# Kernel tuning notes

Measured on AMD Instinct MI355X. Metric: run time of the kernel, lower is better.

Reference implementation:

```python
import jax, jax.numpy as jnp
import numpy as np

B, S, D = 1, 2048, 1024
H, DK = 16, 64
DFF, E, K = 4096, 8, 2
EPS = float(np.finfo(np.float32).eps)  # torch nn.RMSNorm default eps = finfo.eps


def setup_inputs() -> dict:
    key = jax.random.key(0)
    ks = jax.random.split(key, 8)
    s = 0.02
    return {
        "x": jax.random.normal(ks[0], (B, S, D), jnp.float32),
        "qkv_w": jax.random.normal(ks[1], (3 * D, D), jnp.float32) * s,
        "out_w": jax.random.normal(ks[2], (D, D), jnp.float32) * s,
        "router_w": jax.random.normal(ks[3], (E, D), jnp.float32) * s,
        "w1": jax.random.normal(ks[4], (E, DFF, D), jnp.float32) * s,
        "w2": jax.random.normal(ks[5], (E, D, DFF), jnp.float32) * s,
        "norm1_w": jnp.ones((D,), jnp.float32),
        "norm2_w": jnp.ones((D,), jnp.float32),
    }


def _rmsnorm(x, w):
    return x * jax.lax.rsqrt(jnp.mean(x * x, axis=-1, keepdims=True) + EPS) * w


def _rope(x):
    # x: [B, S, H, dk]; rotate-half RoPE as in RotaryPositionalEmbedding
    dk = x.shape[-1]
    inv_freq = 1.0 / (10000.0 ** (jnp.arange(0, dk, 2, dtype=jnp.float32) / dk))
    t = jnp.arange(x.shape[1], dtype=jnp.float32)
    freqs = t[:, None] * inv_freq[None, :]          # [S, dk/2]
    cos = jnp.cos(freqs)[None, :, None, :]
    sin = jnp.sin(freqs)[None, :, None, :]
    x1, x2 = jnp.split(x, 2, axis=-1)
    return jnp.concatenate([x1 * cos - x2 * sin, x2 * cos + x1 * sin], axis=-1)


def _block(x, qkv_w, out_w, router_w, w1, w2, norm1_w, norm2_w):
    Bv, Sv, Dv = x.shape
    # --- attention with RoPE (causal, eval mode) ---
    h = _rmsnorm(x, norm1_w)
    qkv = (h @ qkv_w.T).reshape(Bv, Sv, 3, H, DK)
    q, k, v = qkv[:, :, 0], qkv[:, :, 1], qkv[:, :, 2]   # [B,S,H,dk]
    q = _rope(q)
    k = _rope(k)
    scores = jnp.einsum('bshd,bthd->bhst', q, k) / np.float32(np.sqrt(DK))
    causal = jnp.tril(jnp.ones((Sv, Sv), dtype=bool))
    scores = jnp.where(causal, scores, jnp.float32(-jnp.inf))
    attn = jax.nn.softmax(scores, axis=-1)
    o = jnp.einsum('bhst,bthd->bshd', attn, v).reshape(Bv, Sv, Dv)
    x = x + o @ out_w.T
    # --- MoE with top-k routing ---
    h2 = _rmsnorm(x, norm2_w).reshape(-1, Dv)            # [T, D]
    logits = h2 @ router_w.T                             # [T, E]
    probs = jax.nn.softmax(logits, axis=-1)
    top_p, top_i = jax.lax.top_k(probs, K)               # [T, K]
    top_p = top_p / jnp.sum(top_p, axis=-1, keepdims=True)
    T = h2.shape[0]
    # dense per-token per-expert combine weights (same math as masked loop)
    w_dense = jnp.zeros((T, E), h2.dtype).at[jnp.arange(T)[:, None], top_i].add(top_p)
    hid = jax.nn.gelu(jnp.einsum('td,efd->etf', h2, w1), approximate=False)  # [E,T,DFF]
    eo = jnp.einsum('etf,edf->etd', hid, w2)                                  # [E,T,D]
    moe = jnp.einsum('etd,te->td', eo, w_dense).reshape(Bv, Sv, Dv)
    aux_loss = E * jnp.sum(jnp.mean(probs, axis=0) ** 2)
    return x + moe, aux_loss


def reference(x, qkv_w, out_w, router_w, w1, w2, norm1_w, norm2_w):
    return _block(x, qkv_w, out_w, router_w, w1, w2, norm1_w, norm2_w)
```

## Files before the change

### kernel.cpp

```cpp
#include <hip/hip_runtime.h>
#include <cstdint>
#include <math.h>

typedef float f32x4 __attribute__((ext_vector_type(4)));
typedef __bf16 bf16x8 __attribute__((ext_vector_type(8)));
typedef unsigned short us4 __attribute__((ext_vector_type(4)));

#define DEV static __device__ __forceinline__

DEV unsigned short f2bf(float f){
  union { __bf16 h; unsigned short u; } cv; cv.h = (__bf16)f; return cv.u;
}
DEV float bf2f(unsigned short u){ return __uint_as_float((unsigned int)u << 16); }

DEV void gload16(const void* g, void* l){
  __builtin_amdgcn_global_load_lds((__attribute__((address_space(1))) void*)g,
                                   (__attribute__((address_space(3))) void*)l, 16, 0, 0);
}

__global__ __launch_bounds__(256) void rmsnorm_kernel(const float* __restrict__ x, const float* __restrict__ w,
    unsigned short* __restrict__ ob){
  int t = blockIdx.x, tid = threadIdx.x;
  float4 xv = *(const float4*)(x + (long long)t*1024 + tid*4);
  float ss = xv.x*xv.x + xv.y*xv.y + xv.z*xv.z + xv.w*xv.w;
  for (int m=32;m;m>>=1) ss += __shfl_xor(ss,m);
  __shared__ float lds[4];
  if ((tid&63)==0) lds[tid>>6] = ss;
  __syncthreads();
  float tot = lds[0]+lds[1]+lds[2]+lds[3];
  float inv = rsqrtf(tot*(1.0f/1024.0f) + 1.1920928955078125e-07f);
  float4 wv = *(const float4*)(w + tid*4);
  us4 rb = { f2bf(xv.x*inv*wv.x), f2bf(xv.y*inv*wv.y), f2bf(xv.z*inv*wv.z), f2bf(xv.w*inv*wv.w) };
  *(us4*)&ob[(long long)t*1024 + tid*4] = rb;
}

__global__ __launch_bounds__(256) void rmsnorm2_kernel(const float* __restrict__ xp, int ksn, long long kstride,
    const float* __restrict__ w, float* __restrict__ x1, unsigned short* __restrict__ hb, float* __restrict__ hf){
  int t = blockIdx.x, tid = threadIdx.x;
  long long b = (long long)t*1024 + tid*4;
  float4 xv = {0.f,0.f,0.f,0.f};
  for (int ks=0; ks<ksn; ++ks){
    float4 a = *(const float4*)(xp + ks*kstride + b);
    xv.x+=a.x; xv.y+=a.y; xv.z+=a.z; xv.w+=a.w;
  }
  *(float4*)(x1 + b) = xv;
  float ss = xv.x*xv.x + xv.y*xv.y + xv.z*xv.z + xv.w*xv.w;
  for (int m=32;m;m>>=1) ss += __shfl_xor(ss,m);
  __shared__ float lds[4];
  if ((tid&63)==0) lds[tid>>6] = ss;
  __syncthreads();
  float tot = lds[0]+lds[1]+lds[2]+lds[3];
  float inv = rsqrtf(tot*(1.0f/1024.0f) + 1.1920928955078125e-07f);
  float4 wv = *(const float4*)(w + tid*4);
  float r0 = xv.x*inv*wv.x, r1 = xv.y*inv*wv.y, r2 = xv.z*inv*wv.z, r3 = xv.w*inv*wv.w;
  us4 rb = { f2bf(r0), f2bf(r1), f2bf(r2), f2bf(r3) };
  *(us4*)&hb[b] = rb;
  float4 rf; rf.x=r0; rf.y=r1; rf.z=r2; rf.w=r3;
  *(float4*)(hf + b) = rf;
}

template<int EPI, bool GATHER>
__global__ __launch_bounds__(256) void gemm_bt(
    const unsigned short* __restrict__ A, int lda,
    const float* __restrict__ Bw, long long bstride, int ldb,
    int M, int N, int K, int KS, long long ksoff,
    const int* __restrict__ counts, const int* __restrict__ offs,
    const int* __restrict__ tok_list, const float* __restrict__ wgt,
    const float* __restrict__ resid,
    float* __restrict__ Cf, unsigned short* __restrict__ Cb, int ldc)
{
  const int z = blockIdx.z;
  const int e = z / KS, ks = z - e*KS;
  const int Me = counts ? counts[e] : M;
  const int by = blockIdx.y;
  if (by * 128 >= Me) return;
  const int rbase = offs ? offs[e] : 0;
  const int bx = blockIdx.x;
  const float* B = Bw + (long long)e * bstride;
  const int kn = K / KS;
  const int kbeg = ks * kn;
  const int nt = kn >> 5;

  __shared__ __align__(16) char smem[49152];

  const int tid = threadIdx.x, lane = tid & 63, w = tid >> 6;
  const int wr = w >> 1, wc = w & 1;

  const unsigned short* asrc[2];
  #pragma unroll
  for (int i = 0; i < 2; ++i){
    int G = tid + i*256;
    int R = G >> 2, c = G & 3;
    int cg = c ^ ((R>>1)&3);
    int lr = by*128 + R; if (lr >= Me) lr = Me-1;
    int li = rbase + lr;
    int ar = GATHER ? (tok_list[li] >> 1) : li;
    asrc[i] = A + (long long)ar * lda + kbeg + cg*8;
  }
  const float* bsrc[4];
  #pragma unroll
  for (int i = 0; i < 4; ++i){
    int G = tid + i*256;
    int R = G >> 3, c = G & 7;
    int cg = c ^ (R & 7);
    bsrc[i] = B + (long long)(bx*128 + R) * ldb + kbeg + cg*4;
  }

  f32x4 acc[4][4] = {};

  auto stage = [&](int b, int kof){
    char* s = smem + b*24576;
    #pragma unroll
    for (int i = 0; i < 2; ++i) gload16(asrc[i] + kof, s + (i*256 + w*64)*16);
    #pragma unroll
    for (int i = 0; i < 4; ++i) gload16(bsrc[i] + kof, s + 8192 + (i*256 + w*64)*16);
  };

  stage(0, 0);
  __syncthreads();

  for (int t = 0; t < nt; ++t){
    int cur = t & 1;
    if (t + 1 < nt) stage(cur ^ 1, (t+1)*32);
    const char* abase = smem + cur*24576;
    const char* bbase = abase + 8192;
    bf16x8 af[4], bfr[4];
    #pragma unroll
    for (int m=0;m<4;++m){
      int R = wr*64 + m*16 + (lane&15);
      int c = (lane>>4) ^ ((R>>1)&3);
      af[m] = *(const bf16x8*)(abase + R*64 + c*16);
    }
    #pragma unroll
    for (int n=0;n<4;++n){
      int R = wc*64 + n*16 + (lane&15);
      int c0 = ((lane>>4)*2) ^ (R&7);
      int c1 = c0 ^ 1;
      f32x4 v0 = *(const f32x4*)(bbase + R*128 + c0*16);
      f32x4 v1 = *(const f32x4*)(bbase + R*128 + c1*16);
      bf16x8 tt;
      tt[0]=(__bf16)v0[0]; tt[1]=(__bf16)v0[1]; tt[2]=(__bf16)v0[2]; tt[3]=(__bf16)v0[3];
      tt[4]=(__bf16)v1[0]; tt[5]=(__bf16)v1[1]; tt[6]=(__bf16)v1[2]; tt[7]=(__bf16)v1[3];
      bfr[n] = tt;
    }
    #pragma unroll
    for (int m=0;m<4;++m)
      #pragma unroll
      for (int n=0;n<4;++n)
        acc[m][n] = __builtin_amdgcn_mfma_f32_16x16x32_bf16(af[m], bfr[n], acc[m][n], 0, 0, 0);
    __syncthreads();
  }

  #pragma unroll
  for (int m=0;m<4;++m){
    #pragma unroll
    for (int r=0;r<4;++r){
      int lr = by*128 + wr*64 + m*16 + 4*(lane>>4) + r;
      if (lr >= Me) continue;
      #pragma unroll
      for (int n=0;n<4;++n){
        int col = bx*128 + wc*64 + n*16 + (lane&15);
        float v = acc[m][n][r];
        if constexpr (EPI == 1){
          if (ks == 0) v += resid[(long long)lr*ldc + col];
          Cf[ks*ksoff + (long long)lr*ldc + col] = v;
        } else if constexpr (EPI == 2){
          float g = 0.5f * v * (1.0f + erff(v * 0.70710678118654752f));
          Cb[(long long)(rbase+lr)*ldc + col] = f2bf(g);
        } else if constexpr (EPI == 3){
          int gi = rbase + lr;
          int ts = tok_list[gi];
          Cf[ks*ksoff + (long long)ts*ldc + col] = v * wgt[gi];
        } else {
          Cb[(long long)lr*ldc + col] = f2bf(v);
        }
      }
    }
  }
}

__global__ __launch_bounds__(256) void rope_kernel(const unsigned short* __restrict__ qkvb,
    unsigned short* __restrict__ q, unsigned short* __restrict__ k){
  int t = blockIdx.x, tid = threadIdx.x;
  const unsigned short* row = qkvb + (long long)t*3072;
  #pragma unroll
  for (int u2=0; u2<2; ++u2){
    int pid = tid + u2*256;
    int hh = pid >> 5, j = pid & 31;
    float invf = __expf(-(float)j * 0.28782313662425575f);
    float fr = (float)t * invf;
    float sn, cs;
    __sincosf(fr, &sn, &cs);
    int base = hh*64 + j;
    long long ob_ = (long long)t*1024 + base;
    float a = bf2f(row[base]), b = bf2f(row[base+32]);
    q[ob_]    = f2bf(a*cs - b*sn);
    q[ob_+32] = f2bf(b*cs + a*sn);
    a = bf2f(row[1024+base]); b = bf2f(row[1024+base+32]);
    k[ob_]    = f2bf(a*cs - b*sn);
    k[ob_+32] = f2bf(b*cs + a*sn);
  }
}

__global__ __launch_bounds__(256) void attn_kernel(
    const unsigned short* __restrict__ Q,
    const unsigned short* __restrict__ K,
    const unsigned short* __restrict__ V, int ldv,
    unsigned short* __restrict__ O)
{
  const int bx = blockIdx.x, h = blockIdx.y;
  const int q0 = bx*64;
  const int tid = threadIdx.x, lane = tid&63, w = tid>>6;

  __shared__ __align__(16) unsigned short Ks[64*64];
  __shared__ __align__(16) unsigned short Vs[64*64];
  __shared__ __align__(16) unsigned short Ps[4*16*64];
  unsigned short* Pw = Ps + w*1024;

  const int qrow = q0 + w*16 + (lane&15);
  bf16x8 aq[2];
  #pragma unroll
  for (int kk=0;kk<2;++kk)
    aq[kk] = *(const bf16x8*)&Q[(long long)qrow*1024 + h*64 + 32*kk + 8*(lane>>4)];

  f32x4 o[4] = {};
  float Mx[4] = {-INFINITY,-INFINITY,-INFINITY,-INFINITY};
  float Ls[4] = {0.f,0.f,0.f,0.f};

  const int row_g = q0 + w*16 + 4*(lane>>4);
  const int nt = bx + 1;
  for (int it = 0; it < nt; ++it){
    int k0 = it*64;
    #pragma unroll
    for (int i=0;i<2;++i){
      int seg = 4*i + w;
      int row = seg*8 + (lane>>3);
      int cs = (lane&7) ^ (row&7);
      gload16(&K[(long long)(k0+row)*1024 + h*64 + cs*8], &Ks[seg*512]);
      gload16(&V[(long long)(k0+row)*ldv  + h*64 + cs*8], &Vs[seg*512]);
    }
    __syncthreads();
    f32x4 st[4];
    #pragma unroll
    for (int kt=0;kt<4;++kt){
      f32x4 s = {0.f,0.f,0.f,0.f};
      #pragma unroll
      for (int kk=0;kk<2;++kk){
        int R = kt*16 + (lane&15);
        int ch = ((lane>>4)+4*kk) ^ (R&7);
        bf16x8 bk = *(const bf16x8*)&Ks[R*64 + ch*8];
        s = __builtin_amdgcn_mfma_f32_16x16x32_bf16(aq[kk], bk, s, 0,0,0);
      }
      st[kt] = s;
    }
    #pragma unroll
    for (int kt=0;kt<4;++kt){
      int col = k0 + kt*16 + (lane&15);
      #pragma unroll
      for (int r=0;r<4;++r){
        float vv = st[kt][r]*0.125f;
        st[kt][r] = (col <= row_g + r) ? vv : -INFINITY;
      }
    }
    float sf[4];
    #pragma unroll
    for (int r=0;r<4;++r){
      float mx = fmaxf(fmaxf(st[0][r],st[1][r]),fmaxf(st[2][r],st[3][r]));
      mx = fmaxf(mx, __shfl_xor(mx,1));
      mx = fmaxf(mx, __shfl_xor(mx,2));
      mx = fmaxf(mx, __shfl_xor(mx,4));
      mx = fmaxf(mx, __shfl_xor(mx,8));
      float mn = fmaxf(Mx[r], mx);
      float sc = __expf(Mx[r]-mn);
      Mx[r]=mn; sf[r]=sc;
      float ls=0.f;
      #pragma unroll
      for (int kt=0;kt<4;++kt){ float pp = __expf(st[kt][r]-mn); st[kt][r]=pp; ls+=pp; }
      Ls[r] = Ls[r]*sc + ls;
    }
    #pragma unroll
    for (int dt=0;dt<4;++dt)
      #pragma unroll
      for (int r=0;r<4;++r) o[dt][r] *= sf[r];
    #pragma unroll
    for (int kt=0;kt<4;++kt)
      #pragma unroll
      for (int r=0;r<4;++r){
        int prow = 4*(lane>>4)+r, pcol = kt*16+(lane&15);
        int byteoff = (prow*128 + pcol*2) ^ ((prow&7)<<4);
        *(unsigned short*)((char*)Pw + byteoff) = f2bf(st[kt][r]);
      }
    bf16x8 pa[2];
    #pragma unroll
    for (int kk=0;kk<2;++kk){
      int pr = lane&15;
      int ch = ((lane>>4)+4*kk) ^ (pr&7);
      pa[kk] = *(const bf16x8*)&Pw[pr*64 + ch*8];
    }
    #pragma unroll
    for (int dt=0;dt<4;++dt){
      #pragma unroll
      for (int kk=0;kk<2;++kk){
        union { unsigned short u[8]; bf16x8 v; } Ub;
        #pragma unroll
        for (int j=0;j<8;++j){
          int kr = 32*kk + 8*(lane>>4) + j;
          int d = dt*16 + (lane&15);
          int byteoff = (kr*128 + d*2) ^ ((kr&7)<<4);
          Ub.u[j] = *(const unsigned short*)((const char*)Vs + byteoff);
        }
        o[dt] = __builtin_amdgcn_mfma_f32_16x16x32_bf16(pa[kk], Ub.v, o[dt], 0,0,0);
      }
    }
    __syncthreads();
  }
  #pragma unroll
  for (int r=0;r<4;++r){
    float l = Ls[r];
    l += __shfl_xor(l,1); l += __shfl_xor(l,2); l += __shfl_xor(l,4); l += __shfl_xor(l,8);
    Ls[r] = 1.0f / l;
  }
  #pragma unroll
  for (int dt=0;dt<4;++dt)
    #pragma unroll
    for (int r=0;r<4;++r){
      float vv = o[dt][r]*Ls[r];
      int rg = row_g + r;
      O[(long long)rg*1024 + h*64 + dt*16 + (lane&15)] = f2bf(vv);
    }
}

__global__ __launch_bounds__(256) void router_kernel(const float* __restrict__ h2f, const float* __restrict__ rw,
    float* __restrict__ probs, int* __restrict__ tope, float* __restrict__ topw, int* __restrict__ counts){
  int t = blockIdx.x, tid = threadIdx.x;
  float4 hv = *(const float4*)(h2f + (long long)t*1024 + tid*4);
  float pe[8];
  #pragma unroll
  for (int e2=0;e2<8;++e2){
    float4 wv = *(const float4*)(rw + e2*1024 + tid*4);
    pe[e2] = hv.x*wv.x + hv.y*wv.y + hv.z*wv.z + hv.w*wv.w;
  }
  __shared__ float lds[32];
  #pragma unroll
  for (int e2=0;e2<8;++e2){
    float v = pe[e2];
    for (int m=32;m;m>>=1) v += __shfl_xor(v,m);
    if ((tid&63)==0) lds[(tid>>6)*8+e2] = v;
  }
  __syncthreads();
  if (tid==0){
    float lg[8], pp[8];
    #pragma unroll
    for (int e2=0;e2<8;++e2) lg[e2] = lds[e2]+lds[8+e2]+lds[16+e2]+lds[24+e2];
    float mx = lg[0];
    for (int e2=1;e2<8;++e2) mx = fmaxf(mx, lg[e2]);
    float s = 0.f;
    for (int e2=0;e2<8;++e2){ pp[e2] = __expf(lg[e2]-mx); s += pp[e2]; }
    float inv = 1.0f/s;
    int i0 = 0;
    for (int e2=1;e2<8;++e2) if (pp[e2] > pp[i0]) i0 = e2;
    int i1 = (i0==0)?1:0;
    for (int e2=0;e2<8;++e2) if (e2!=i0 && pp[e2] > pp[i1]) i1 = e2;
    for (int e2=0;e2<8;++e2) probs[t*8+e2] = pp[e2]*inv;
    float p0 = pp[i0], p1 = pp[i1], wsum = p0+p1;
    tope[t*2] = i0; tope[t*2+1] = i1;
    topw[t*2] = p0/wsum; topw[t*2+1] = p1/wsum;
    atomicAdd(&counts[i0],1); atomicAdd(&counts[i1],1);
  }
}

__global__ void init_kernel(int* counts, int* cursor){
  int i = threadIdx.x;
  if (i<8){ counts[i]=0; cursor[i]=0; }
}

__global__ void prefix_kernel(const int* counts, int* offs){
  if (threadIdx.x==0){
    int a=0;
    for (int e2=0;e2<8;++e2){ offs[e2]=a; a+=counts[e2]; }
  }
}

__global__ void scatter_kernel(const int* __restrict__ tope, const float* __restrict__ topw,
    const int* __restrict__ offs, int* __restrict__ cursor, int* __restrict__ tok_list, float* __restrict__ wgt){
  int t = blockIdx.x*blockDim.x + threadIdx.x;
  if (t >= 2048) return;
  #pragma unroll
  for (int s=0;s<2;++s){
    int e2 = tope[t*2+s];
    int pos = atomicAdd(&cursor[e2], 1);
    int i = offs[e2] + pos;
    tok_list[i] = t*2+s;
    wgt[i] = topw[t*2+s];
  }
}

__global__ __launch_bounds__(256) void aux_kernel(const float* __restrict__ probs, float* __restrict__ out){
  int tid = threadIdx.x;
  float pe[8] = {0,0,0,0,0,0,0,0};
  for (int t = tid; t < 2048; t += 256){
    #pragma unroll
    for (int e2=0;e2<8;++e2) pe[e2] += probs[t*8+e2];
  }
  __shared__ float lds[32];
  #pragma unroll
  for (int e2=0;e2<8;++e2){
    float v = pe[e2];
    for (int m=32;m;m>>=1) v += __shfl_xor(v,m);
    if ((tid&63)==0) lds[(tid>>6)*8 + e2] = v;
  }
  __syncthreads();
  if (tid==0){
    float aux = 0.f;
    #pragma unroll
    for (int e2=0;e2<8;++e2){
      float mean = (lds[e2]+lds[8+e2]+lds[16+e2]+lds[24+e2]) * (1.0f/2048.0f);
      aux += mean*mean;
    }
    out[2097152] = 8.0f * aux;
  }
}

__global__ __launch_bounds__(256) void final_kernel(const float* __restrict__ x1, const float* __restrict__ slots,
    int ksn, long long kstride, float* __restrict__ out){
  int t = blockIdx.x, tid = threadIdx.x;
  long long b = (long long)t*1024 + tid*4;
  float4 a = *(const float4*)(x1 + b);
  long long s = (long long)t*2048 + tid*4;
  for (int ks=0; ks<ksn; ++ks){
    float4 s0 = *(const float4*)(slots + ks*kstride + s);
    float4 s1 = *(const float4*)(slots + ks*kstride + s + 1024);
    a.x += s0.x + s1.x; a.y += s0.y + s1.y; a.z += s0.z + s1.z; a.w += s0.w + s1.w;
  }
  *(float4*)(out + b) = a;
}

extern "C" void kernel_launch(void* const* d_in, const int* in_sizes, int n_in,
                              void* d_out, int out_size, void* d_ws, size_t ws_size,
                              hipStream_t stream)
{
  (void)in_sizes; (void)n_in; (void)out_size;
  const float* x    = (const float*)d_in[0];
  const float* qkvw = (const float*)d_in[1];
  const float* outw = (const float*)d_in[2];
  const float* rw   = (const float*)d_in[3];
  const float* w1   = (const float*)d_in[4];
  const float* w2   = (const float*)d_in[5];
  const float* n1w  = (const float*)d_in[6];
  const float* n2w  = (const float*)d_in[7];
  float* out = (float*)d_out;

  char* base = (char*)d_ws;
  const size_t MB = 1ull<<20;
  const bool big = ws_size >= 150*MB;
  const int KSO = big ? 4 : 2;
  const int KSW = big ? 4 : 2;

  unsigned short* h_b  = (unsigned short*)(base + 0*MB);
  unsigned short* qb   = (unsigned short*)(base + 4*MB);
  unsigned short* kb   = (unsigned short*)(base + 8*MB);
  unsigned short* ob   = (unsigned short*)(base + 12*MB);
  unsigned short* qkvb = (unsigned short*)(base + 16*MB);
  unsigned short* hid  = (unsigned short*)(base + 0*MB);

  float *x1p, *h2f, *slots, *x1;
  unsigned short* h2b;
  char* small_;
  if (big){
    x1p   = (float*)(base + 32*MB);
    h2f   = (float*)(base + 64*MB);
    slots = (float*)(base + 72*MB);
    x1    = (float*)(base + 136*MB);
    h2b   = (unsigned short*)(base + 144*MB);
    small_ = base + 148*MB;
  } else {
    x1p   = (float*)(base + 32*MB);
    h2f   = (float*)(base + 48*MB);
    slots = (float*)(base + 32*MB);
    x1    = (float*)(base + 64*MB);
    h2b   = (unsigned short*)(base + 72*MB);
    small_ = base + 76*MB;
  }
  float* probs = (float*)(small_);
  int*   tope  = (int*)(small_ + 256*1024);
  float* topw  = (float*)(small_ + 512*1024);
  int*   tok_list = (int*)(small_ + 768*1024);
  float* wgt   = (float*)(small_ + 1024*1024);
  int*   counts= (int*)(small_ + 1536*1024);
  int*   offs  = (int*)(small_ + 1536*1024 + 256);
  int*   cursor= (int*)(small_ + 1536*1024 + 512);

  init_kernel<<<1,64,0,stream>>>(counts, cursor);
  rmsnorm_kernel<<<2048,256,0,stream>>>(x, n1w, h_b);
  gemm_bt<4,false><<<dim3(24,16,1),256,0,stream>>>(h_b,1024, qkvw,0,1024, 2048,3072,1024, 1,0,
      nullptr,nullptr,nullptr,nullptr,nullptr, nullptr,qkvb,3072);
  rope_kernel<<<2048,256,0,stream>>>(qkvb, qb, kb);
  attn_kernel<<<dim3(32,16),256,0,stream>>>(qb, kb, qkvb+2048, 3072, ob);
  gemm_bt<1,false><<<dim3(8,16,KSO),256,0,stream>>>(ob,1024, outw,0,1024, 2048,1024,1024, KSO,(long long)2048*1024,
      nullptr,nullptr,nullptr,nullptr, x, x1p,nullptr,1024);
  rmsnorm2_kernel<<<2048,256,0,stream>>>(x1p, KSO, (long long)2048*1024, n2w, x1, h2b, h2f);
  router_kernel<<<2048,256,0,stream>>>(h2f, rw, probs, tope, topw, counts);
  prefix_kernel<<<1,64,0,stream>>>(counts, offs);
  scatter_kernel<<<8,256,0,stream>>>(tope, topw, offs, cursor, tok_list, wgt);
  gemm_bt<2,true><<<dim3(32,16,8),256,0,stream>>>(h2b,1024, w1,(long long)4096*1024,1024, 2048,4096,1024, 1,0,
      counts,offs,tok_list,nullptr,nullptr, nullptr,hid,4096);
  gemm_bt<3,false><<<dim3(8,16,8*KSW),256,0,stream>>>(hid,4096, w2,(long long)4096*1024,4096, 2048,1024,4096, KSW,(long long)4096*1024,
      counts,offs,tok_list,wgt,nullptr, slots,nullptr,1024);
  aux_kernel<<<1,256,0,stream>>>(probs, out);
  final_kernel<<<2048,256,0,stream>>>(x1, slots, KSW, (long long)4096*1024, out);
}
```

Measured before the change: 452.9 us.

## Replace LDS-staged GEMM with direct global-load streaming GEMM and XCD-aware block remap

The double-buffered LDS GEMM, which used async global-to-LDS loads and a barrier per k-step, is replaced by a kernel where each wave loads its A and B fragments straight from global memory into registers. The output tile changes from 128x128 to 64x256, with each wave owning a 64-column strip. Block indices are remapped so consecutive tiles land on the same XCD, which should improve L2 locality. This removes the LDS traffic and barriers, but it gives up on-chip sharing of operands between waves, so the kernel now depends on L1/L2 hit rates and more global load instructions.

Result: slower. 867.6 us (+91.6%).

```diff
diff --git a/kernel.cpp b/kernel.cpp
--- a/kernel.cpp
+++ b/kernel.cpp
@@ -60,7 +60,7 @@
 }
 
 template<int EPI, bool GATHER>
-__global__ __launch_bounds__(256) void gemm_bt(
+__global__ __launch_bounds__(256) void gemm_stream(
     const unsigned short* __restrict__ A, int lda,
     const float* __restrict__ Bw, long long bstride, int ldb,
     int M, int N, int K, int KS, long long ksoff,
@@ -69,75 +69,56 @@
     const float* __restrict__ resid,
     float* __restrict__ Cf, unsigned short* __restrict__ Cb, int ldc)
 {
-  const int z = blockIdx.z;
+  const int gx = gridDim.x, gy = gridDim.y;
+  int flat = blockIdx.x + gx*(blockIdx.y + gy*blockIdx.z);
+  int nwg = gx*gy*gridDim.z;
+  int q = nwg >> 3, r = nwg & 7;
+  int xcd = flat & 7, p = flat >> 3;
+  int nf = (xcd < r ? xcd*(q+1) : r*(q+1) + (xcd-r)*q) + p;
+  const int by = nf % gx;
+  int rest = nf / gx;
+  const int bx = rest % gy;
+  const int z  = rest / gy;
+
   const int e = z / KS, ks = z - e*KS;
   const int Me = counts ? counts[e] : M;
-  const int by = blockIdx.y;
-  if (by * 128 >= Me) return;
+  if (by * 64 >= Me) return;
   const int rbase = offs ? offs[e] : 0;
-  const int bx = blockIdx.x;
   const float* B = Bw + (long long)e * bstride;
-  const int kn = K / KS;
-  const int kbeg = ks * kn;
-  const int nt = kn >> 5;
-
-  __shared__ __align__(16) char smem[49152];
-
-  const int tid = threadIdx.x, lane = tid & 63, w = tid >> 6;
-  const int wr = w >> 1, wc = w & 1;
-
-  const unsigned short* asrc[2];
-  #pragma unroll
-  for (int i = 0; i < 2; ++i){
-    int G = tid + i*256;
-    int R = G >> 2, c = G & 3;
-    int cg = c ^ ((R>>1)&3);
-    int lr = by*128 + R; if (lr >= Me) lr = Me-1;
+  const int kbeg = ks * (K/KS);
+  const int nt = (K/KS) >> 5;
+
+  const int lane = threadIdx.x & 63, w = threadIdx.x >> 6;
+  const int l15 = lane & 15, l4 = lane >> 4;
+
+  const unsigned short* arow[4];
+  #pragma unroll
+  for (int m=0;m<4;++m){
+    int lr = by*64 + m*16 + l15; if (lr >= Me) lr = Me-1;
     int li = rbase + lr;
     int ar = GATHER ? (tok_list[li] >> 1) : li;
-    asrc[i] = A + (long long)ar * lda + kbeg + cg*8;
-  }
-  const float* bsrc[4];
-  #pragma unroll
-  for (int i = 0; i < 4; ++i){
-    int G = tid + i*256;
-    int R = G >> 3, c = G & 7;
-    int cg = c ^ (R & 7);
-    bsrc[i] = B + (long long)(bx*128 + R) * ldb + kbeg + cg*4;
+    arow[m] = A + (long long)ar*lda + kbeg + l4*8;
+  }
+  const float* brow[4];
+  #pragma unroll
+  for (int n=0;n<4;++n){
+    int R = bx*256 + w*64 + n*16 + l15;
+    brow[n] = B + (long long)R*ldb + kbeg + l4*8;
   }
 
   f32x4 acc[4][4] = {};
 
-  auto stage = [&](int b, int kof){
-    char* s = smem + b*24576;
-    #pragma unroll
-    for (int i = 0; i < 2; ++i) gload16(asrc[i] + kof, s + (i*256 + w*64)*16);
-    #pragma unroll
-    for (int i = 0; i < 4; ++i) gload16(bsrc[i] + kof, s + 8192 + (i*256 + w*64)*16);
-  };
-
-  stage(0, 0);
-  __syncthreads();
-
+  #pragma unroll 2
   for (int t = 0; t < nt; ++t){
-    int cur = t & 1;
-    if (t + 1 < nt) stage(cur ^ 1, (t+1)*32);
-    const char* abase = smem + cur*24576;
-    const char* bbase = abase + 8192;
-    bf16x8 af[4], bfr[4];
-    #pragma unroll
-    for (int m=0;m<4;++m){
-      int R = wr*64 + m*16 + (lane&15);
-      int c = (lane>>4) ^ ((R>>1)&3);
-      af[m] = *(const bf16x8*)(abase + R*64 + c*16);
-    }
+    const int k0 = t*32;
+    bf16x8 af[4];
+    #pragma unroll
+    for (int m=0;m<4;++m) af[m] = *(const bf16x8*)(arow[m] + k0);
+    bf16x8 bfr[4];
     #pragma unroll
     for (int n=0;n<4;++n){
-      int R = wc*64 + n*16 + (lane&15);
-      int c0 = ((lane>>4)*2) ^ (R&7);
-      int c1 = c0 ^ 1;
-      f32x4 v0 = *(const f32x4*)(bbase + R*128 + c0*16);
-      f32x4 v1 = *(const f32x4*)(bbase + R*128 + c1*16);
+      f32x4 v0 = *(const f32x4*)(brow[n] + k0);
+      f32x4 v1 = *(const f32x4*)(brow[n] + k0 + 4);
       bf16x8 tt;
       tt[0]=(__bf16)v0[0]; tt[1]=(__bf16)v0[1]; tt[2]=(__bf16)v0[2]; tt[3]=(__bf16)v0[3];
       tt[4]=(__bf16)v1[0]; tt[5]=(__bf16)v1[1]; tt[6]=(__bf16)v1[2]; tt[7]=(__bf16)v1[3];
@@ -148,19 +129,18 @@
       #pragma unroll
       for (int n=0;n<4;++n)
         acc[m][n] = __builtin_amdgcn_mfma_f32_16x16x32_bf16(af[m], bfr[n], acc[m][n], 0, 0, 0);
-    __syncthreads();
   }
 
   #pragma unroll
   for (int m=0;m<4;++m){
     #pragma unroll
-    for (int r=0;r<4;++r){
-      int lr = by*128 + wr*64 + m*16 + 4*(lane>>4) + r;
+    for (int r2=0;r2<4;++r2){
+      int lr = by*64 + m*16 + 4*l4 + r2;
       if (lr >= Me) continue;
       #pragma unroll
       for (int n=0;n<4;++n){
-        int col = bx*128 + wc*64 + n*16 + (lane&15);
-        float v = acc[m][n][r];
+        int col = bx*256 + w*64 + n*16 + l15;
+        float v = acc[m][n][r2];
         if constexpr (EPI == 1){
           if (ks == 0) v += resid[(long long)lr*ldc + col];
           Cf[ks*ksoff + (long long)lr*ldc + col] = v;
@@ -492,19 +472,19 @@
 
   init_kernel<<<1,64,0,stream>>>(counts, cursor);
   rmsnorm_kernel<<<2048,256,0,stream>>>(x, n1w, h_b);
-  gemm_bt<4,false><<<dim3(24,16,1),256,0,stream>>>(h_b,1024, qkvw,0,1024, 2048,3072,1024, 1,0,
+  gemm_stream<4,false><<<dim3(32,12,1),256,0,stream>>>(h_b,1024, qkvw,0,1024, 2048,3072,1024, 1,0,
       nullptr,nullptr,nullptr,nullptr,nullptr, nullptr,qkvb,3072);
   rope_kernel<<<2048,256,0,stream>>>(qkvb, qb, kb);
   attn_kernel<<<dim3(32,16),256,0,stream>>>(qb, kb, qkvb+2048, 3072, ob);
-  gemm_bt<1,false><<<dim3(8,16,KSO),256,0,stream>>>(ob,1024, outw,0,1024, 2048,1024,1024, KSO,(long long)2048*1024,
+  gemm_stream<1,false><<<dim3(32,4,KSO),256,0,stream>>>(ob,1024, outw,0,1024, 2048,1024,1024, KSO,(long long)2048*1024,
       nullptr,nullptr,nullptr,nullptr, x, x1p,nullptr,1024);
   rmsnorm2_kernel<<<2048,256,0,stream>>>(x1p, KSO, (long long)2048*1024, n2w, x1, h2b, h2f);
   router_kernel<<<2048,256,0,stream>>>(h2f, rw, probs, tope, topw, counts);
   prefix_kernel<<<1,64,0,stream>>>(counts, offs);
   scatter_kernel<<<8,256,0,stream>>>(tope, topw, offs, cursor, tok_list, wgt);
-  gemm_bt<2,true><<<dim3(32,16,8),256,0,stream>>>(h2b,1024, w1,(long long)4096*1024,1024, 2048,4096,1024, 1,0,
+  gemm_stream<2,true><<<dim3(32,16,8),256,0,stream>>>(h2b,1024, w1,(long long)4096*1024,1024, 2048,4096,1024, 1,0,
       counts,offs,tok_list,nullptr,nullptr, nullptr,hid,4096);
-  gemm_bt<3,false><<<dim3(8,16,8*KSW),256,0,stream>>>(hid,4096, w2,(long long)4096*1024,4096, 2048,1024,4096, KSW,(long long)4096*1024,
+  gemm_stream<3,false><<<dim3(32,4,8*KSW),256,0,stream>>>(hid,4096, w2,(long long)4096*1024,4096, 2048,1024,4096, KSW,(long long)4096*1024,
       counts,offs,tok_list,wgt,nullptr, slots,nullptr,1024);
   aux_kernel<<<1,256,0,stream>>>(probs, out);
   final_kernel<<<2048,256,0,stream>>>(x1, slots, KSW, (long long)4096*1024, out);
```

## Pre-convert weights to bf16 and use a bf16-bf16 GEMM with K=64 tiles

Applied to the files above, without the earlier changes.

Adds a conversion kernel that turns the fp32 weight matrices into bf16 in workspace before each GEMM. The GEMM then loads bf16 for both operands with 64-wide K tiles, instead of staging fp32 B and converting in registers. This is meant to cut the LDS footprint and conversion ALU work inside the GEMM. In exchange it adds extra full-weight passes each call, and replaces double-buffered staging with a single buffer and two barriers per step. It also fixes the split-K factors and the workspace layout, dropping the small-workspace fallback.

Result: faster. 436.5 us (-3.6%).

```diff
diff --git a/kernel.cpp b/kernel.cpp
--- a/kernel.cpp
+++ b/kernel.cpp
@@ -5,6 +5,7 @@
 typedef float f32x4 __attribute__((ext_vector_type(4)));
 typedef __bf16 bf16x8 __attribute__((ext_vector_type(8)));
 typedef unsigned short us4 __attribute__((ext_vector_type(4)));
+typedef unsigned short us8 __attribute__((ext_vector_type(8)));
 
 #define DEV static __device__ __forceinline__
 
@@ -16,6 +17,17 @@
 DEV void gload16(const void* g, void* l){
   __builtin_amdgcn_global_load_lds((__attribute__((address_space(1))) void*)g,
                                    (__attribute__((address_space(3))) void*)l, 16, 0, 0);
+}
+
+__global__ __launch_bounds__(256) void conv_kernel(const float* __restrict__ src,
+    unsigned short* __restrict__ dst, int n8){
+  int i = blockIdx.x*256 + threadIdx.x;
+  if (i >= n8) return;
+  float4 a = ((const float4*)src)[2*i];
+  float4 b = ((const float4*)src)[2*i+1];
+  us8 o = { f2bf(a.x), f2bf(a.y), f2bf(a.z), f2bf(a.w),
+            f2bf(b.x), f2bf(b.y), f2bf(b.z), f2bf(b.w) };
+  ((us8*)dst)[i] = o;
 }
 
 __global__ __launch_bounds__(256) void rmsnorm_kernel(const float* __restrict__ x, const float* __restrict__ w,
@@ -60,9 +72,9 @@
 }
 
 template<int EPI, bool GATHER>
-__global__ __launch_bounds__(256) void gemm_bt(
+__global__ __launch_bounds__(256) void gemm_bb(
     const unsigned short* __restrict__ A, int lda,
-    const float* __restrict__ Bw, long long bstride, int ldb,
+    const unsigned short* __restrict__ Bb, long long bstride, int ldb,
     int M, int N, int K, int KS, long long ksoff,
     const int* __restrict__ counts, const int* __restrict__ offs,
     const int* __restrict__ tok_list, const float* __restrict__ wgt,
@@ -76,91 +88,74 @@
   if (by * 128 >= Me) return;
   const int rbase = offs ? offs[e] : 0;
   const int bx = blockIdx.x;
-  const float* B = Bw + (long long)e * bstride;
+  const unsigned short* B = Bb + (long long)e * bstride;
   const int kn = K / KS;
   const int kbeg = ks * kn;
-  const int nt = kn >> 5;
-
-  __shared__ __align__(16) char smem[49152];
+
+  __shared__ __align__(16) unsigned short As[128*64];
+  __shared__ __align__(16) unsigned short Bs[128*64];
 
   const int tid = threadIdx.x, lane = tid & 63, w = tid >> 6;
   const int wr = w >> 1, wc = w & 1;
-
-  const unsigned short* asrc[2];
-  #pragma unroll
-  for (int i = 0; i < 2; ++i){
-    int G = tid + i*256;
-    int R = G >> 2, c = G & 3;
-    int cg = c ^ ((R>>1)&3);
+  const int l15 = lane & 15, l4 = lane >> 4;
+
+  const unsigned short* asrc[4];
+  const unsigned short* bsrc[4];
+  #pragma unroll
+  for (int j=0;j<4;++j){
+    int G = j*256 + tid;
+    int R = G >> 3, c = G & 7;
+    int sc = c ^ (R & 7);
     int lr = by*128 + R; if (lr >= Me) lr = Me-1;
     int li = rbase + lr;
     int ar = GATHER ? (tok_list[li] >> 1) : li;
-    asrc[i] = A + (long long)ar * lda + kbeg + cg*8;
-  }
-  const float* bsrc[4];
-  #pragma unroll
-  for (int i = 0; i < 4; ++i){
-    int G = tid + i*256;
-    int R = G >> 3, c = G & 7;
-    int cg = c ^ (R & 7);
-    bsrc[i] = B + (long long)(bx*128 + R) * ldb + kbeg + cg*4;
+    asrc[j] = A + (long long)ar*lda + kbeg + sc*8;
+    bsrc[j] = B + (long long)(bx*128 + R)*ldb + kbeg + sc*8;
   }
 
   f32x4 acc[4][4] = {};
 
-  auto stage = [&](int b, int kof){
-    char* s = smem + b*24576;
-    #pragma unroll
-    for (int i = 0; i < 2; ++i) gload16(asrc[i] + kof, s + (i*256 + w*64)*16);
-    #pragma unroll
-    for (int i = 0; i < 4; ++i) gload16(bsrc[i] + kof, s + 8192 + (i*256 + w*64)*16);
-  };
-
-  stage(0, 0);
-  __syncthreads();
-
-  for (int t = 0; t < nt; ++t){
-    int cur = t & 1;
-    if (t + 1 < nt) stage(cur ^ 1, (t+1)*32);
-    const char* abase = smem + cur*24576;
-    const char* bbase = abase + 8192;
-    bf16x8 af[4], bfr[4];
-    #pragma unroll
-    for (int m=0;m<4;++m){
-      int R = wr*64 + m*16 + (lane&15);
-      int c = (lane>>4) ^ ((R>>1)&3);
-      af[m] = *(const bf16x8*)(abase + R*64 + c*16);
-    }
-    #pragma unroll
-    for (int n=0;n<4;++n){
-      int R = wc*64 + n*16 + (lane&15);
-      int c0 = ((lane>>4)*2) ^ (R&7);
-      int c1 = c0 ^ 1;
-      f32x4 v0 = *(const f32x4*)(bbase + R*128 + c0*16);
-      f32x4 v1 = *(const f32x4*)(bbase + R*128 + c1*16);
-      bf16x8 tt;
-      tt[0]=(__bf16)v0[0]; tt[1]=(__bf16)v0[1]; tt[2]=(__bf16)v0[2]; tt[3]=(__bf16)v0[3];
-      tt[4]=(__bf16)v1[0]; tt[5]=(__bf16)v1[1]; tt[6]=(__bf16)v1[2]; tt[7]=(__bf16)v1[3];
-      bfr[n] = tt;
-    }
-    #pragma unroll
-    for (int m=0;m<4;++m)
-      #pragma unroll
-      for (int n=0;n<4;++n)
-        acc[m][n] = __builtin_amdgcn_mfma_f32_16x16x32_bf16(af[m], bfr[n], acc[m][n], 0, 0, 0);
+  for (int k0 = 0; k0 < kn; k0 += 64){
     __syncthreads();
+    #pragma unroll
+    for (int j=0;j<4;++j){
+      gload16(asrc[j] + k0, &As[(j*256+tid)*8]);
+      gload16(bsrc[j] + k0, &Bs[(j*256+tid)*8]);
+    }
+    __syncthreads();
+    #pragma unroll
+    for (int kk=0;kk<2;++kk){
+      bf16x8 af[4], bfr[4];
+      #pragma unroll
+      for (int m=0;m<4;++m){
+        int R = wr*64 + m*16 + l15;
+        int c = (l4 + 4*kk) ^ (R&7);
+        af[m] = *(const bf16x8*)&As[R*64 + c*8];
+      }
+      #pragma unroll
+      for (int n=0;n<4;++n){
+        int R = wc*64 + n*16 + l15;
+        int c = (l4 + 4*kk) ^ (R&7);
+        bfr[n] = *(const bf16x8*)&Bs[R*64 + c*8];
+      }
+      #pragma unroll
+      for (int m=0;m<4;++m)
+        #pragma unroll
+        for (int n=0;n<4;++n)
+          acc[m][n] = __builtin_amdgcn_mfma_f32_16x16x32_bf16(af[m], bfr[n], acc[m][n], 0, 0, 0);
+    }
   }
 
   #pragma unroll
   for (int m=0;m<4;++m){
     #pragma unroll
-    for (int r=0;r<4;++r){
-      int lr = by*128 + wr*64 + m*16 + 4*(lane>>4) + r;
+    for (int r2=0;r2<4;++r2){
+      int lr = by*128 + wr*64 + m*16 + 4*l4 + r2;
       if (lr >= Me) continue;
       #pragma unroll
       for (int n=0;n<4;++n){
-        int col = bx*128 + wc*64 + n*16 + (lane&15);
-        float v = acc[m][n][r];
+        int col = bx*128 + wc*64 + n*16 + l15;
+        float v = acc[m][n][r2];
         if constexpr (EPI == 1){
           if (ks == 0) v += resid[(long long)lr*ldc + col];
           Cf[ks*ksoff + (long long)lr*ldc + col] = v;
@@ -439,7 +434,7 @@
                               void* d_out, int out_size, void* d_ws, size_t ws_size,
                               hipStream_t stream)
 {
-  (void)in_sizes; (void)n_in; (void)out_size;
+  (void)in_sizes; (void)n_in; (void)out_size; (void)ws_size;
   const float* x    = (const float*)d_in[0];
   const float* qkvw = (const float*)d_in[1];
   const float* outw = (const float*)d_in[2];
@@ -452,9 +447,8 @@
 
   char* base = (char*)d_ws;
   const size_t MB = 1ull<<20;
-  const bool big = ws_size >= 150*MB;
-  const int KSO = big ? 4 : 2;
-  const int KSW = big ? 4 : 2;
+  const int KSO = 4;
+  const int KSW = 2;
 
   unsigned short* h_b  = (unsigned short*)(base + 0*MB);
   unsigned short* qb   = (unsigned short*)(base + 4*MB);
@@ -463,24 +457,17 @@
   unsigned short* qkvb = (unsigned short*)(base + 16*MB);
   unsigned short* hid  = (unsigned short*)(base + 0*MB);
 
-  float *x1p, *h2f, *slots, *x1;
-  unsigned short* h2b;
-  char* small_;
-  if (big){
-    x1p   = (float*)(base + 32*MB);
-    h2f   = (float*)(base + 64*MB);
-    slots = (float*)(base + 72*MB);
-    x1    = (float*)(base + 136*MB);
-    h2b   = (unsigned short*)(base + 144*MB);
-    small_ = base + 148*MB;
-  } else {
-    x1p   = (float*)(base + 32*MB);
-    h2f   = (float*)(base + 48*MB);
-    slots = (float*)(base + 32*MB);
-    x1    = (float*)(base + 64*MB);
-    h2b   = (unsigned short*)(base + 72*MB);
-    small_ = base + 76*MB;
-  }
+  unsigned short* wbq = (unsigned short*)(base + 32*MB);
+  unsigned short* wbo = (unsigned short*)(base + 40*MB);
+  unsigned short* wb  = (unsigned short*)(base + 32*MB);
+
+  float* x1p   = (float*)(base + 96*MB);
+  float* slots = (float*)(base + 96*MB);
+  float* h2f   = (float*)(base + 128*MB);
+  float* x1    = (float*)(base + 136*MB);
+  unsigned short* h2b = (unsigned short*)(base + 144*MB);
+  char* small_ = base + 148*MB;
+
   float* probs = (float*)(small_);
   int*   tope  = (int*)(small_ + 256*1024);
   float* topw  = (float*)(small_ + 512*1024);
@@ -492,19 +479,23 @@
 
   init_kernel<<<1,64,0,stream>>>(counts, cursor);
   rmsnorm_kernel<<<2048,256,0,stream>>>(x, n1w, h_b);
-  gemm_bt<4,false><<<dim3(24,16,1),256,0,stream>>>(h_b,1024, qkvw,0,1024, 2048,3072,1024, 1,0,
+  conv_kernel<<<1536,256,0,stream>>>(qkvw, wbq, 3*1024*1024/8);
+  conv_kernel<<<512,256,0,stream>>>(outw, wbo, 1024*1024/8);
+  gemm_bb<4,false><<<dim3(24,16,1),256,0,stream>>>(h_b,1024, wbq,0,1024, 2048,3072,1024, 1,0,
       nullptr,nullptr,nullptr,nullptr,nullptr, nullptr,qkvb,3072);
   rope_kernel<<<2048,256,0,stream>>>(qkvb, qb, kb);
   attn_kernel<<<dim3(32,16),256,0,stream>>>(qb, kb, qkvb+2048, 3072, ob);
-  gemm_bt<1,false><<<dim3(8,16,KSO),256,0,stream>>>(ob,1024, outw,0,1024, 2048,1024,1024, KSO,(long long)2048*1024,
+  gemm_bb<1,false><<<dim3(8,16,KSO),256,0,stream>>>(ob,1024, wbo,0,1024, 2048,1024,1024, KSO,(long long)2048*1024,
       nullptr,nullptr,nullptr,nullptr, x, x1p,nullptr,1024);
   rmsnorm2_kernel<<<2048,256,0,stream>>>(x1p, KSO, (long long)2048*1024, n2w, x1, h2b, h2f);
   router_kernel<<<2048,256,0,stream>>>(h2f, rw, probs, tope, topw, counts);
   prefix_kernel<<<1,64,0,stream>>>(counts, offs);
   scatter_kernel<<<8,256,0,stream>>>(tope, topw, offs, cursor, tok_list, wgt);
-  gemm_bt<2,true><<<dim3(32,16,8),256,0,stream>>>(h2b,1024, w1,(long long)4096*1024,1024, 2048,4096,1024, 1,0,
+  conv_kernel<<<16384,256,0,stream>>>(w1, wb, 32*1024*1024/8);
+  gemm_bb<2,true><<<dim3(32,16,8),256,0,stream>>>(h2b,1024, wb,(long long)4096*1024,1024, 2048,4096,1024, 1,0,
       counts,offs,tok_list,nullptr,nullptr, nullptr,hid,4096);
-  gemm_bt<3,false><<<dim3(8,16,8*KSW),256,0,stream>>>(hid,4096, w2,(long long)4096*1024,4096, 2048,1024,4096, KSW,(long long)4096*1024,
+  conv_kernel<<<16384,256,0,stream>>>(w2, wb, 32*1024*1024/8);
+  gemm_bb<3,false><<<dim3(8,16,8*KSW),256,0,stream>>>(hid,4096, wb,(long long)4096*1024,4096, 2048,1024,4096, KSW,(long long)4096*1024,
       counts,offs,tok_list,wgt,nullptr, slots,nullptr,1024);
   aux_kernel<<<1,256,0,stream>>>(probs, out);
   final_kernel<<<2048,256,0,stream>>>(x1, slots, KSW, (long long)4096*1024, out);
```
